# Optimization experiments

Hardware: AMD Instinct MI355X
Metric: run time of the kernel (lower is better)

The kernel has to match this reference:

```python
import jax, jax.numpy as jnp
import numpy as np

IMG = 512
B = 4
NA = 3          # anchors per location
NC = 3          # classes
K = 512         # pre-NMS top-k per image per level (<= smallest level anchor count 768)
STRIDES = [4, 8, 16, 32]
MIN_S = [0.01, 0.02, 0.03, 0.04]
MAX_S = [0.06, 0.08, 0.10, 0.12]
W_SC = [0.8, 0.9, 1.0, 1.1]
H_SC = [1.0, 1.2, 1.4, 1.6]
CONF_T = 0.15
NMS_T = 0.5
STD = 0.2       # box_delta_stds (means are 0)


def make_anchors(stride):
    H = IMG // stride
    c = (np.arange(H) + 0.5) * stride
    cy, cx = np.meshgrid(c, c, indexing='ij')           # [H, W]
    sizes = stride * 4.0 * (2.0 ** (np.arange(NA) / 3.0))  # [A]
    cx = np.broadcast_to(cx, (NA, H, H))
    cy = np.broadcast_to(cy, (NA, H, H))
    s = sizes[:, None, None]
    # A-major, then H, W -- matches permute(0,1,3,4,2).reshape flattening
    anc = np.stack([cx - s / 2, cy - s / 2, cx + s / 2, cy + s / 2], -1).reshape(-1, 4)
    return jnp.asarray(anc, jnp.float32)


def setup_inputs() -> dict:
    key = jax.random.key(0)
    ks = jax.random.split(key, 8)
    inp = {}
    for l, s in enumerate(STRIDES):
        H = IMG // s
        inp[f'cls{l}'] = jax.random.normal(ks[2 * l], (B, NA, NC, H, H), jnp.float32)
        inp[f'box{l}'] = jax.random.normal(ks[2 * l + 1], (B, NA, 4, H, H), jnp.float32)
        inp[f'anc{l}'] = make_anchors(s)
    inp['image_size'] = IMG
    return inp


def decode_level(cls, box, anc, lvl, image_size):
    Bc, A, C, H, W = cls.shape
    scores = jax.nn.sigmoid(jnp.transpose(cls, (0, 1, 3, 4, 2)).reshape(Bc, -1, C))  # [B,N,C]
    d = jnp.transpose(box, (0, 1, 3, 4, 2)).reshape(Bc, -1, 4)                        # [B,N,4]
    img = jnp.asarray(image_size, jnp.float32)
    aw = (anc[:, 2] - anc[:, 0]) / img
    ah = (anc[:, 3] - anc[:, 1]) / img
    acx = (anc[:, 0] + anc[:, 2]) * 0.5 / img
    acy = (anc[:, 1] + anc[:, 3]) * 0.5 / img
    fs = 1.0 / STRIDES[lvl]
    dx = jnp.clip(d[..., 0] * STD, -1.0, 1.0) * fs * aw
    dy = jnp.clip(d[..., 1] * STD, -1.0, 1.0) * fs * ah
    cx = jnp.clip(acx + dx, 0.0, 1.0)
    cy = jnp.clip(acy + dy, 0.0, 1.0)
    dw = jnp.clip(d[..., 2] * STD, -2.0, 2.0)
    dh = jnp.clip(d[..., 3] * STD, -2.0, 2.0)
    pw = jnp.clip(aw * W_SC[lvl] * jnp.exp(dw * (0.2 + 0.1 * lvl)), MIN_S[lvl] * 0.8, MAX_S[lvl] * 0.9)
    ph = jnp.clip(ah * H_SC[lvl] * jnp.exp(dh * (0.4 + 0.2 * lvl)), MIN_S[lvl] * 0.8, MAX_S[lvl] * 1.2)
    boxes = jnp.stack([
        jnp.clip(cx - 0.5 * pw, 0.0, 1.0),
        jnp.clip(cy - 0.5 * ph, 0.0, 1.0),
        jnp.clip(cx + 0.5 * pw, 0.0, 1.0),
        jnp.clip(cy + 0.5 * ph, 0.0, 1.0)], -1)                                       # [B,N,4]
    ms = scores.max(-1)
    mc = scores.argmax(-1)
    w = boxes[..., 2] - boxes[..., 0]
    h = boxes[..., 3] - boxes[..., 1]
    valid = (ms > CONF_T) & (w > MIN_S[lvl] * 0.5) & (h > MIN_S[lvl] * 0.5) \
            & (w < MAX_S[lvl] * 2.0) & (h < MAX_S[lvl] * 2.0)
    # pre-NMS top-k on (masked) scores
    sort_key = jnp.where(valid, ms, -1.0)
    _, idx = jax.lax.top_k(sort_key, K)                                               # [B,K]
    boxes_k = jnp.take_along_axis(boxes, idx[..., None], 1)
    scores_k = jnp.take_along_axis(ms, idx, 1)
    labels_k = jnp.take_along_axis(mc, idx, 1)
    valid_k = jnp.take_along_axis(valid, idx, 1)
    return boxes_k, scores_k, labels_k, valid_k


def pairwise_iou(b):
    area = (b[:, 2] - b[:, 0]) * (b[:, 3] - b[:, 1])
    lt = jnp.maximum(b[:, None, :2], b[None, :, :2])
    rb = jnp.minimum(b[:, None, 2:], b[None, :, 2:])
    wh = jnp.clip(rb - lt, 0.0)
    inter = wh[..., 0] * wh[..., 1]
    return inter / (area[:, None] + area[None, :] - inter + 1e-9)


def nms_keep(boxes, valid):
    # boxes sorted by descending score; sequential greedy NMS
    iou = pairwise_iou(boxes)                 # [K,K]
    rank = jnp.arange(K)
    def body(i, keep):
        overlap = jnp.max(jnp.where((rank < i) & keep, iou[i], 0.0))
        return keep.at[i].set(valid[i] & (overlap <= NMS_T))
    return jax.lax.fori_loop(0, K, body, jnp.zeros((K,), bool))


def reference(cls0, box0, anc0, cls1, box1, anc1, cls2, box2, anc2, cls3, box3, anc3, image_size):
    levels = [(cls0, box0, anc0), (cls1, box1, anc1), (cls2, box2, anc2), (cls3, box3, anc3)]
    outs = [decode_level(c, b, a, l, image_size) for l, (c, b, a) in enumerate(levels)]
    boxes = jnp.stack([o[0] for o in outs], 1)    # [B, L, K, 4]
    scores = jnp.stack([o[1] for o in outs], 1)   # [B, L, K]
    labels = jnp.stack([o[2] for o in outs], 1)   # [B, L, K]
    valid = jnp.stack([o[3] for o in outs], 1)    # [B, L, K]
    keep = jax.vmap(jax.vmap(nms_keep))(boxes, valid)
    boxes = jnp.where(keep[..., None], boxes, 0.0)
    scores = jnp.where(keep, scores, 0.0)
    labels = jnp.where(keep, labels + 1, 0)       # torch code returns labels + 1
    return boxes, scores, labels, keep
```

## Files before the change

kernel.cpp:

```cpp
#include <hip/hip_runtime.h>
#include <math.h>

#define K_TOP 512
#define CAND_CAP 3072

struct LvlC {
  int H, lgH, HH, lgHH;
  float fs, wsc, hsc, wex, hex, pwlo, pwhi, phlo, phhi, minwh, maxwh;
};

__device__ const LvlC LVL[4] = {
  {128, 7, 16384, 14, 0.25f,    0.8f, 1.0f, 0.2f, 0.4f, 0.008f, 0.054f, 0.008f, 0.072f, 0.005f, 0.12f},
  { 64, 6,  4096, 12, 0.125f,   0.9f, 1.2f, 0.3f, 0.6f, 0.016f, 0.072f, 0.016f, 0.096f, 0.01f,  0.16f},
  { 32, 5,  1024, 10, 0.0625f,  1.0f, 1.4f, 0.4f, 0.8f, 0.024f, 0.09f,  0.024f, 0.12f,  0.015f, 0.2f },
  { 16, 4,   256,  8, 0.03125f, 1.1f, 1.6f, 0.5f, 1.0f, 0.032f, 0.108f, 0.032f, 0.144f, 0.02f,  0.24f},
};

__device__ const float TSEL[4] = {0.91f, 0.85f, 0.65f, -2.0f};

__device__ unsigned long long g_keys[261120];
__device__ unsigned long long g_cand[261120];
__device__ unsigned           g_unitCnt[1020];
__device__ float4             g_boxes[16 * K_TOP];
__device__ float              g_scores[16 * K_TOP];
__device__ int                g_labels[16 * K_TOP];
__device__ unsigned           g_valid[16 * K_TOP];
__device__ unsigned long long g_masks[16 * K_TOP * 8];

__device__ __forceinline__ void decode_box(const LvlC& L, const float* __restrict__ boxp,
                                           const float* __restrict__ ancp,
                                           int b, int idx, float rimg,
                                           float& x0, float& y0, float& x1, float& y1)
{
#pragma clang fp contract(off)
  int a   = idx >> L.lgHH;
  int rem = idx & (L.HH - 1);
  const float* bp = boxp + (size_t)((b * 3 + a) * 4) * L.HH + rem;
  float d0 = bp[0], d1 = bp[L.HH], d2 = bp[2 * L.HH], d3 = bp[3 * L.HH];
  float4 av = reinterpret_cast<const float4*>(ancp)[idx];
  float a0 = av.x, a1 = av.y, a2 = av.z, a3 = av.w;
  float aw  = (a2 - a0) * rimg;
  float ah  = (a3 - a1) * rimg;
  float acx = (a0 + a2) * 0.5f * rimg;
  float acy = (a1 + a3) * 0.5f * rimg;
  float dx = fminf(fmaxf(d0 * 0.2f, -1.f), 1.f) * L.fs * aw;
  float dy = fminf(fmaxf(d1 * 0.2f, -1.f), 1.f) * L.fs * ah;
  float cx = fminf(fmaxf(acx + dx, 0.f), 1.f);
  float cy = fminf(fmaxf(acy + dy, 0.f), 1.f);
  float dw = fminf(fmaxf(d2 * 0.2f, -2.f), 2.f);
  float dh = fminf(fmaxf(d3 * 0.2f, -2.f), 2.f);
  float pw = fminf(fmaxf(aw * L.wsc * expf(dw * L.wex), L.pwlo), L.pwhi);
  float ph = fminf(fmaxf(ah * L.hsc * expf(dh * L.hex), L.phlo), L.phhi);
  x0 = fminf(fmaxf(cx - 0.5f * pw, 0.f), 1.f);
  y0 = fminf(fmaxf(cy - 0.5f * ph, 0.f), 1.f);
  x1 = fminf(fmaxf(cx + 0.5f * pw, 0.f), 1.f);
  y1 = fminf(fmaxf(cy + 0.5f * ph, 0.f), 1.f);
}

__device__ __forceinline__ void seg_map(int blk, int& b, int& l, int& base, int& iblk)
{
  b = blk / 255;
  int rb = blk - b * 255;
  if (rb < 192)      { l = 0; iblk = rb;       base = 0;     }
  else if (rb < 240) { l = 1; iblk = rb - 192; base = 49152; }
  else if (rb < 252) { l = 2; iblk = rb - 240; base = 61440; }
  else               { l = 3; iblk = rb - 252; base = 64512; }
}

__global__ __launch_bounds__(256) void dc_kernel(
    const float* __restrict__ cls0, const float* __restrict__ box0, const float* __restrict__ anc0,
    const float* __restrict__ cls1, const float* __restrict__ box1, const float* __restrict__ anc1,
    const float* __restrict__ cls2, const float* __restrict__ box2, const float* __restrict__ anc2,
    const float* __restrict__ cls3, const float* __restrict__ box3, const float* __restrict__ anc3,
    const int* __restrict__ imgp)
{
  __shared__ unsigned wcnt[4];
  int unit = (int)blockIdx.x;
  int tid = (int)threadIdx.x;
  int wid = tid >> 6, lane = tid & 63;
  int b, l, base, iblk;
  seg_map(unit, b, l, base, iblk);
  int i = iblk * 256 + tid;

  const float *cls, *boxp, *ancp;
  switch (l) {
    case 0:  cls = cls0; boxp = box0; ancp = anc0; break;
    case 1:  cls = cls1; boxp = box1; ancp = anc1; break;
    case 2:  cls = cls2; boxp = box2; ancp = anc2; break;
    default: cls = cls3; boxp = box3; ancp = anc3; break;
  }
  LvlC L = LVL[l];
  float rimg = 1.0f / (float)(*imgp);

  int a   = i >> L.lgHH;
  int rem = i & (L.HH - 1);
  const float* cp = cls + (size_t)((b * 3 + a) * 3) * L.HH + rem;
  float c0 = cp[0], c1 = cp[L.HH], c2 = cp[2 * L.HH];
  float m = c0; int mc = 0;
  if (c1 > m) { m = c1; mc = 1; }
  if (c2 > m) { m = c2; mc = 2; }
  float ms = 1.f / (1.f + expf(-m));

  float x0, y0, x1, y1;
  decode_box(L, boxp, ancp, b, i, rimg, x0, y0, x1, y1);
  float w = x1 - x0, h = y1 - y0;
  bool valid = (ms > 0.15f) && (w > L.minwh) && (h > L.minwh) && (w < L.maxwh) && (h < L.maxwh);

  float sk = valid ? ms : -1.0f;
  unsigned u = __float_as_uint(sk);
  unsigned ascu  = (u & 0x80000000u) ? ~u : (u | 0x80000000u);
  unsigned descu = ~ascu;
  unsigned long long key = ((unsigned long long)descu << 32)
                         | ((unsigned long long)(unsigned)i << 16)
                         | ((unsigned)mc << 8) | (valid ? 1u : 0u);
  g_keys[(size_t)b * 65280 + base + i] = key;

  bool take = (sk >= TSEL[l]);
  unsigned long long bm = __ballot(take);
  if (lane == 0) wcnt[wid] = (unsigned)__popcll(bm);
  __syncthreads();
  if (take) {
    unsigned off = 0;
    for (int w2 = 0; w2 < wid; ++w2) off += wcnt[w2];
    off += (unsigned)__popcll(bm & ((1ull << lane) - 1ull));
    g_cand[(size_t)unit * 256 + off] = key;
  }
  if (tid == 0) g_unitCnt[unit] = wcnt[0] + wcnt[1] + wcnt[2] + wcnt[3];
}

__global__ __launch_bounds__(512) void sel_kernel(
    const float* __restrict__ box0, const float* __restrict__ anc0,
    const float* __restrict__ box1, const float* __restrict__ anc1,
    const float* __restrict__ box2, const float* __restrict__ anc2,
    const float* __restrict__ box3, const float* __restrict__ anc3,
    const int* __restrict__ imgp)
{
  __shared__ unsigned long long scand[CAND_CAP];
  __shared__ unsigned long long skey[K_TOP];
  __shared__ unsigned long long skey2[K_TOP];
  __shared__ unsigned hist[8][256];
  __shared__ unsigned upref[256];
  __shared__ unsigned waveSum[8];
  __shared__ unsigned long long shPrefix;
  __shared__ unsigned long long shKth;
  __shared__ unsigned shBelow, shCnt, shTotal, shBucketCnt, sBC;

  int seg = (int)blockIdx.x;
  int b = seg >> 2, l = seg & 3;
  int tid = (int)threadIdx.x;
  const int nt = 512;
  int wid = tid >> 6, lane = tid & 63;

  const int nArr[4]    = {49152, 12288, 3072, 768};
  const int baseArr[4] = {0, 49152, 61440, 64512};
  const int nuArr[4]   = {192, 48, 12, 3};
  const int fuArr[4]   = {0, 192, 240, 252};
  int N = nArr[l];
  int nu = nuArr[l];
  int firstU = b * 255 + fuArr[l];
  const unsigned long long* kp = g_keys + (size_t)b * 65280 + baseArr[l];

  if (tid == 0) { shPrefix = 0ull; shBelow = 0u; shCnt = 0u; sBC = 0u; shBucketCnt = 0xFFFFFFFFu; }

  unsigned c = (tid < nu) ? g_unitCnt[firstU + tid] : 0u;
  unsigned incl = c;
  for (int off = 1; off < 64; off <<= 1) {
    unsigned n = __shfl_up(incl, off);
    if (lane >= off) incl += n;
  }
  if (lane == 63) waveSum[wid] = incl;
  __syncthreads();
  if (tid < 256) {
    unsigned add = 0;
    for (int w2 = 0; w2 < wid; ++w2) add += waveSum[w2];
    if (tid < nu) upref[tid] = incl - c + add;
  }
  if (tid == 0) shTotal = waveSum[0] + waveSum[1] + waveSum[2] + waveSum[3];
  __syncthreads();

  unsigned total = shTotal;
  bool useCand = (total >= K_TOP && total <= CAND_CAP);
  int M = useCand ? (int)total : N;

  if (useCand) {
    for (int f = tid; f < (int)total; f += nt) {
      int lo = 0, hi = nu - 1;
      while (lo < hi) {
        int mid = (lo + hi + 1) >> 1;
        if ((int)upref[mid] <= f) lo = mid; else hi = mid - 1;
      }
      scand[f] = g_cand[(size_t)(firstU + lo) * 256 + (unsigned)(f - (int)upref[lo])];
    }
  }
  __syncthreads();

  int lastShift = 16;
  for (int r = 0; r < 6; ++r) {
    int shift = 56 - 8 * r;
    for (int v = tid; v < 8 * 256; v += nt) ((unsigned*)hist)[v] = 0u;
    __syncthreads();
    unsigned long long pref = shPrefix;
    unsigned below = shBelow;
    unsigned long long hiMask = (r == 0) ? 0ull : (~0ull << (64 - 8 * r));
    for (int t = tid; t < M; t += nt) {
      unsigned long long k = useCand ? scand[t] : kp[t];
      if ((k & hiMask) == (pref & hiMask))
        atomicAdd(&hist[wid][(unsigned)((k >> shift) & 0xFF)], 1u);
    }
    __syncthreads();
    unsigned s = 0, incl2 = 0;
    if (tid < 256) {
#pragma unroll
      for (int w2 = 0; w2 < 8; ++w2) s += hist[w2][tid];
      incl2 = s;
    }
    for (int off = 1; off < 64; off <<= 1) {
      unsigned n = __shfl_up(incl2, off);
      if (lane >= off) incl2 += n;
    }
    if (lane == 63) waveSum[wid] = incl2;
    __syncthreads();
    if (tid < 256) {
      unsigned add = 0;
      for (int w2 = 0; w2 < wid; ++w2) add += waveSum[w2];
      unsigned inclT = incl2 + add;
      unsigned exclT = inclT - s;
      if (below + exclT < K_TOP && below + inclT >= K_TOP) {
        shBelow = below + exclT;
        shPrefix = pref | ((unsigned long long)(unsigned)tid << shift);
        shBucketCnt = s;
      }
    }
    __syncthreads();
    if (shBucketCnt <= (unsigned)K_TOP) { lastShift = shift; break; }
  }

  {
    unsigned long long pmask = ~0ull << lastShift;
    unsigned long long pref = shPrefix;
    for (int t = tid; t < M; t += nt) {
      unsigned long long k = useCand ? scand[t] : kp[t];
      bool take = ((k & pmask) == pref);
      unsigned long long bm = __ballot(take);
      unsigned bp = 0;
      if (lane == 0 && bm) bp = atomicAdd(&sBC, (unsigned)__popcll(bm));
      bp = __shfl(bp, 0);
      if (take) skey[bp + (unsigned)__popcll(bm & ((1ull << lane) - 1ull))] = k;
    }
    __syncthreads();
    unsigned cnt = sBC;
    unsigned rneed = K_TOP - shBelow;
    if (tid < (int)cnt) {
      unsigned long long mykey = skey[tid];
      int rank = 0;
      for (unsigned j = 0; j < cnt; ++j) rank += (skey[j] < mykey) ? 1 : 0;
      if (rank == (int)(rneed - 1)) shKth = mykey;
    }
    __syncthreads();
  }
  unsigned long long kth = shKth;

  for (int t = tid; t < M; t += nt) {
    unsigned long long k = useCand ? scand[t] : kp[t];
    bool take = (k <= kth);
    unsigned long long bm = __ballot(take);
    unsigned bp = 0;
    if (lane == 0 && bm) bp = atomicAdd(&shCnt, (unsigned)__popcll(bm));
    bp = __shfl(bp, 0);
    if (take) skey[bp + (unsigned)__popcll(bm & ((1ull << lane) - 1ull))] = k;
  }
  __syncthreads();

  {
    unsigned long long mykey = skey[tid];
    int rank = 0;
#pragma unroll 8
    for (int j = 0; j < K_TOP; ++j) rank += (skey[j] < mykey) ? 1 : 0;
    skey2[rank] = mykey;
  }
  __syncthreads();

  const float *boxp, *ancp;
  switch (l) {
    case 0:  boxp = box0; ancp = anc0; break;
    case 1:  boxp = box1; ancp = anc1; break;
    case 2:  boxp = box2; ancp = anc2; break;
    default: boxp = box3; ancp = anc3; break;
  }
  LvlC L = LVL[l];
  float rimg = 1.0f / (float)(*imgp);
  {
    unsigned long long key = skey2[tid];
    int idx = (int)((key >> 16) & 0xFFFFull);
    unsigned descu = (unsigned)(key >> 32);
    unsigned ascu  = ~descu;
    unsigned u = (ascu & 0x80000000u) ? (ascu & 0x7FFFFFFFu) : ~ascu;
    float x0, y0, x1, y1;
    decode_box(L, boxp, ancp, b, idx, rimg, x0, y0, x1, y1);
    int o = seg * K_TOP + tid;
    float4 bb; bb.x = x0; bb.y = y0; bb.z = x1; bb.w = y1;
    g_boxes[o] = bb;
    g_scores[o] = __uint_as_float(u);
    g_labels[o] = (int)((key >> 8) & 0xFFull);
    g_valid[o]  = (unsigned)(key & 1ull);
  }
}

__global__ __launch_bounds__(256) void mask_kernel()
{
#pragma clang fp contract(off)
  int blk = (int)blockIdx.x;
  int seg = blk >> 5;
  int wid = (int)threadIdx.x >> 6;
  int lane = (int)threadIdx.x & 63;
  int waveInSeg = (blk & 31) * 4 + wid;
  const float4* bb = g_boxes + seg * K_TOP;
  unsigned long long* mseg = g_masks + (size_t)seg * K_TOP * 8;

  float4 bj[8]; float aj[8];
#pragma unroll
  for (int c = 0; c < 8; ++c) {
    bj[c] = bb[c * 64 + lane];
    aj[c] = (bj[c].z - bj[c].x) * (bj[c].w - bj[c].y);
  }
#pragma unroll
  for (int rr = 0; rr < 4; ++rr) {
    int r = waveInSeg * 4 + rr;
    float4 br = bb[r];
    float ar_ = (br.z - br.x) * (br.w - br.y);
#pragma unroll
    for (int c = 0; c < 8; ++c) {
      float ltx = fmaxf(br.x, bj[c].x), lty = fmaxf(br.y, bj[c].y);
      float rbx = fminf(br.z, bj[c].z), rby = fminf(br.w, bj[c].w);
      float ww = fmaxf(rbx - ltx, 0.f), hh = fmaxf(rby - lty, 0.f);
      float inter = ww * hh;
      float iou = inter / (ar_ + aj[c] - inter + 1e-9f);
      unsigned long long bal = __ballot(iou > 0.5f);
      if (lane == 0) mseg[c * K_TOP + r] = bal;
    }
  }
}

__global__ __launch_bounds__(512) void scan_kernel(float* __restrict__ out)
{
  __shared__ unsigned long long sMaskT[8 * K_TOP];
  __shared__ unsigned long long keepWords[8];
  __shared__ unsigned sChanged;

  int seg = (int)blockIdx.x;
  int tid = (int)threadIdx.x;
  int wid = tid >> 6, lane = tid & 63;
  const unsigned long long* mp = g_masks + (size_t)seg * K_TOP * 8;
#pragma unroll
  for (int w = 0; w < 8; ++w) sMaskT[w * K_TOP + tid] = mp[w * K_TOP + tid];
  bool valid = g_valid[seg * K_TOP + tid] != 0u;

  unsigned long long myWord = __ballot(valid);
  if (lane == 0) keepWords[wid] = myWord;
  __syncthreads();

  for (int it = 0; it < 513; ++it) {
    unsigned long long sup = 0ull;
    for (int w = 0; w < wid; ++w)
      sup |= sMaskT[w * K_TOP + tid] & keepWords[w];
    sup |= sMaskT[wid * K_TOP + tid] & keepWords[wid] & ((1ull << lane) - 1ull);
    bool nk = valid && (sup == 0ull);
    unsigned long long nw = __ballot(nk);
    __syncthreads();
    if (tid == 0) sChanged = 0u;
    __syncthreads();
    if (lane == 0) {
      if (nw != keepWords[wid]) sChanged = 1u;
      keepWords[wid] = nw;
    }
    __syncthreads();
    if (sChanged == 0u) break;
  }

  int o = seg * K_TOP + tid;
  bool keep = (keepWords[wid] >> lane) & 1ull;
  float4 bx = g_boxes[o];
  float4 ob;
  ob.x = keep ? bx.x : 0.f;
  ob.y = keep ? bx.y : 0.f;
  ob.z = keep ? bx.z : 0.f;
  ob.w = keep ? bx.w : 0.f;
  reinterpret_cast<float4*>(out)[o] = ob;
  out[32768 + o] = keep ? g_scores[o] : 0.f;
  out[40960 + o] = keep ? (float)(g_labels[o] + 1) : 0.f;
  out[49152 + o] = keep ? 1.f : 0.f;
}

extern "C" void kernel_launch(void* const* d_in, const int* in_sizes, int n_in,
                              void* d_out, int out_size, void* d_ws, size_t ws_size,
                              hipStream_t stream)
{
  const float* cls0 = (const float*)d_in[0];
  const float* box0 = (const float*)d_in[1];
  const float* anc0 = (const float*)d_in[2];
  const float* cls1 = (const float*)d_in[3];
  const float* box1 = (const float*)d_in[4];
  const float* anc1 = (const float*)d_in[5];
  const float* cls2 = (const float*)d_in[6];
  const float* box2 = (const float*)d_in[7];
  const float* anc2 = (const float*)d_in[8];
  const float* cls3 = (const float*)d_in[9];
  const float* box3 = (const float*)d_in[10];
  const float* anc3 = (const float*)d_in[11];
  const int*   imgp = (const int*)d_in[12];
  float* out = (float*)d_out;

  (void)d_ws; (void)ws_size;

  dc_kernel<<<1020, 256, 0, stream>>>(cls0, box0, anc0, cls1, box1, anc1,
                                      cls2, box2, anc2, cls3, box3, anc3, imgp);
  sel_kernel<<<16, 512, 0, stream>>>(box0, anc0, box1, anc1, box2, anc2, box3, anc3,
                                     imgp);
  mask_kernel<<<512, 256, 0, stream>>>();
  scan_kernel<<<16, 512, 0, stream>>>(out);
}
```

Baseline: 117.8 us.

## Compact candidates with per-segment global atomics and widen selection blocks

The decode kernel now appends each wave's threshold-passing keys straight into one contiguous per-segment buffer, reserving space with a single global atomic per wave. This replaces the per-block counts, the block-wide barrier, and the prefix-sum plus binary-search gather in the selection kernel. The selection kernel also goes from 512 to 1024 threads with 16 per-wave histograms, to speed up the radix passes on only 16 blocks. In exchange, candidate order becomes nondeterministic and the counters rely on zero-initialised device memory that the selection kernel resets on each call. Segments whose count exceeds the buffer capacity still fall back to scanning all keys.

```diff
diff --git a/kernel.cpp b/kernel.cpp
--- a/kernel.cpp
+++ b/kernel.cpp
@@ -19,8 +19,8 @@
 __device__ const float TSEL[4] = {0.91f, 0.85f, 0.65f, -2.0f};
 
 __device__ unsigned long long g_keys[261120];
-__device__ unsigned long long g_cand[261120];
-__device__ unsigned           g_unitCnt[1020];
+__device__ unsigned long long g_candSeg[16 * CAND_CAP];
+__device__ unsigned           g_candCnt[16];
 __device__ float4             g_boxes[16 * K_TOP];
 __device__ float              g_scores[16 * K_TOP];
 __device__ int                g_labels[16 * K_TOP];
@@ -74,10 +74,9 @@
     const float* __restrict__ cls3, const float* __restrict__ box3, const float* __restrict__ anc3,
     const int* __restrict__ imgp)
 {
-  __shared__ unsigned wcnt[4];
   int unit = (int)blockIdx.x;
   int tid = (int)threadIdx.x;
-  int wid = tid >> 6, lane = tid & 63;
+  int lane = tid & 63;
   int b, l, base, iblk;
   seg_map(unit, b, l, base, iblk);
   int i = iblk * 256 + tid;
@@ -117,18 +116,18 @@
 
   bool take = (sk >= TSEL[l]);
   unsigned long long bm = __ballot(take);
-  if (lane == 0) wcnt[wid] = (unsigned)__popcll(bm);
-  __syncthreads();
+  unsigned cntw = (unsigned)__popcll(bm);
+  unsigned wbase = 0;
+  if (lane == 0 && cntw) wbase = atomicAdd(&g_candCnt[b * 4 + l], cntw);
+  wbase = __shfl(wbase, 0);
   if (take) {
-    unsigned off = 0;
-    for (int w2 = 0; w2 < wid; ++w2) off += wcnt[w2];
-    off += (unsigned)__popcll(bm & ((1ull << lane) - 1ull));
-    g_cand[(size_t)unit * 256 + off] = key;
-  }
-  if (tid == 0) g_unitCnt[unit] = wcnt[0] + wcnt[1] + wcnt[2] + wcnt[3];
-}
-
-__global__ __launch_bounds__(512) void sel_kernel(
+    unsigned slot = wbase + (unsigned)__popcll(bm & ((1ull << lane) - 1ull));
+    if (slot < (unsigned)CAND_CAP)
+      g_candSeg[(b * 4 + l) * CAND_CAP + slot] = key;
+  }
+}
+
+__global__ __launch_bounds__(1024) void sel_kernel(
     const float* __restrict__ box0, const float* __restrict__ anc0,
     const float* __restrict__ box1, const float* __restrict__ anc1,
     const float* __restrict__ box2, const float* __restrict__ anc2,
@@ -138,9 +137,8 @@
   __shared__ unsigned long long scand[CAND_CAP];
   __shared__ unsigned long long skey[K_TOP];
   __shared__ unsigned long long skey2[K_TOP];
-  __shared__ unsigned hist[8][256];
-  __shared__ unsigned upref[256];
-  __shared__ unsigned waveSum[8];
+  __shared__ unsigned hist[16][256];
+  __shared__ unsigned waveSum[16];
   __shared__ unsigned long long shPrefix;
   __shared__ unsigned long long shKth;
   __shared__ unsigned shBelow, shCnt, shTotal, shBucketCnt, sBC;
@@ -148,34 +146,20 @@
   int seg = (int)blockIdx.x;
   int b = seg >> 2, l = seg & 3;
   int tid = (int)threadIdx.x;
-  const int nt = 512;
+  const int nt = 1024;
   int wid = tid >> 6, lane = tid & 63;
 
   const int nArr[4]    = {49152, 12288, 3072, 768};
   const int baseArr[4] = {0, 49152, 61440, 64512};
-  const int nuArr[4]   = {192, 48, 12, 3};
-  const int fuArr[4]   = {0, 192, 240, 252};
   int N = nArr[l];
-  int nu = nuArr[l];
-  int firstU = b * 255 + fuArr[l];
   const unsigned long long* kp = g_keys + (size_t)b * 65280 + baseArr[l];
 
-  if (tid == 0) { shPrefix = 0ull; shBelow = 0u; shCnt = 0u; sBC = 0u; shBucketCnt = 0xFFFFFFFFu; }
-
-  unsigned c = (tid < nu) ? g_unitCnt[firstU + tid] : 0u;
-  unsigned incl = c;
-  for (int off = 1; off < 64; off <<= 1) {
-    unsigned n = __shfl_up(incl, off);
-    if (lane >= off) incl += n;
-  }
-  if (lane == 63) waveSum[wid] = incl;
-  __syncthreads();
-  if (tid < 256) {
-    unsigned add = 0;
-    for (int w2 = 0; w2 < wid; ++w2) add += waveSum[w2];
-    if (tid < nu) upref[tid] = incl - c + add;
-  }
-  if (tid == 0) shTotal = waveSum[0] + waveSum[1] + waveSum[2] + waveSum[3];
+  if (tid == 0) {
+    shPrefix = 0ull; shBelow = 0u; shCnt = 0u; sBC = 0u; shBucketCnt = 0xFFFFFFFFu;
+    unsigned total = g_candCnt[seg];
+    g_candCnt[seg] = 0;
+    shTotal = total;
+  }
   __syncthreads();
 
   unsigned total = shTotal;
@@ -183,21 +167,15 @@
   int M = useCand ? (int)total : N;
 
   if (useCand) {
-    for (int f = tid; f < (int)total; f += nt) {
-      int lo = 0, hi = nu - 1;
-      while (lo < hi) {
-        int mid = (lo + hi + 1) >> 1;
-        if ((int)upref[mid] <= f) lo = mid; else hi = mid - 1;
-      }
-      scand[f] = g_cand[(size_t)(firstU + lo) * 256 + (unsigned)(f - (int)upref[lo])];
-    }
+    for (int f = tid; f < (int)total; f += nt)
+      scand[f] = g_candSeg[seg * CAND_CAP + f];
   }
   __syncthreads();
 
   int lastShift = 16;
   for (int r = 0; r < 6; ++r) {
     int shift = 56 - 8 * r;
-    for (int v = tid; v < 8 * 256; v += nt) ((unsigned*)hist)[v] = 0u;
+    for (int v = tid; v < 16 * 256; v += nt) ((unsigned*)hist)[v] = 0u;
     __syncthreads();
     unsigned long long pref = shPrefix;
     unsigned below = shBelow;
@@ -211,7 +189,7 @@
     unsigned s = 0, incl2 = 0;
     if (tid < 256) {
 #pragma unroll
-      for (int w2 = 0; w2 < 8; ++w2) s += hist[w2][tid];
+      for (int w2 = 0; w2 < 16; ++w2) s += hist[w2][tid];
       incl2 = s;
     }
     for (int off = 1; off < 64; off <<= 1) {
@@ -271,7 +249,7 @@
   }
   __syncthreads();
 
-  {
+  if (tid < K_TOP) {
     unsigned long long mykey = skey[tid];
     int rank = 0;
 #pragma unroll 8
@@ -289,7 +267,7 @@
   }
   LvlC L = LVL[l];
   float rimg = 1.0f / (float)(*imgp);
-  {
+  if (tid < K_TOP) {
     unsigned long long key = skey2[tid];
     int idx = (int)((key >> 16) & 0xFFFFull);
     unsigned descu = (unsigned)(key >> 32);
@@ -414,8 +392,8 @@
 
   dc_kernel<<<1020, 256, 0, stream>>>(cls0, box0, anc0, cls1, box1, anc1,
                                       cls2, box2, anc2, cls3, box3, anc3, imgp);
-  sel_kernel<<<16, 512, 0, stream>>>(box0, anc0, box1, anc1, box2, anc2, box3, anc3,
-                                     imgp);
+  sel_kernel<<<16, 1024, 0, stream>>>(box0, anc0, box1, anc1, box2, anc2, box3, anc3,
+                                      imgp);
   mask_kernel<<<512, 256, 0, stream>>>();
   scan_kernel<<<16, 512, 0, stream>>>(out);
 }
```

New measurement: 147.6 us. +25.3%, slower.
